# Optimization experiments

Measured on AMD Instinct MI355X. Metric: run time of the kernel, lower is better.

The kernel has to match this reference:

```python
import jax, jax.numpy as jnp
import numpy as np

N_SUPPORT = 16384
EMBED_DIM = 1024
MAX_LEVELS = 4
N_CLASSES = 64


def setup_inputs() -> dict:
    key = jax.random.key(0)
    ks = jax.random.split(key, 12)
    D, L = EMBED_DIM, MAX_LEVELS
    s = 0.02
    return {
        "support_features": jax.random.normal(ks[0], (N_SUPPORT, D), jnp.float32),
        "support_labels": jax.random.randint(ks[1], (N_SUPPORT,), 0, N_CLASSES),
        "sp_w1": jax.random.normal(ks[2], (D, D // 2), jnp.float32) * s,
        "sp_b1": jnp.zeros((D // 2,), jnp.float32),
        "sp_w2": jax.random.normal(ks[3], (D // 2, L), jnp.float32) * s,
        "sp_b2": jnp.zeros((L,), jnp.float32),
        "lvl_emb": jax.random.normal(ks[4], (L, 1), jnp.float32) * s,
        "an_w1": jax.random.normal(ks[5], (L, D + 1, D), jnp.float32) * s,
        "an_b1": jnp.zeros((L, D), jnp.float32),
        "an_gamma": jnp.ones((L, D), jnp.float32),
        "an_beta": jnp.zeros((L, D), jnp.float32),
        "an_w2": jax.random.normal(ks[6], (L, D, D), jnp.float32) * s,
        "an_b2": jnp.zeros((L, D), jnp.float32),
        "fu_w1": jax.random.normal(ks[7], (L * D + L, D), jnp.float32) * s,
        "fu_b1": jnp.zeros((D,), jnp.float32),
        "fu_w2": jax.random.normal(ks[8], (D, D), jnp.float32) * s,
        "fu_b2": jnp.zeros((D,), jnp.float32),
        "n_classes": N_CLASSES,
    }


def _forward(support_features, support_labels, sp_w1, sp_b1, sp_w2, sp_b2,
             lvl_emb, an_w1, an_b1, an_gamma, an_beta, an_w2, an_b2,
             fu_w1, fu_b1, fu_w2, fu_b2, n_classes):
    N, D = support_features.shape
    L = an_w1.shape[0]
    # structure predictor on task context (mean pooled support set)
    task_context = support_features.mean(axis=0)
    h = jax.nn.relu(task_context @ sp_w1 + sp_b1)
    acts = jax.nn.sigmoid(h @ sp_w2 + sp_b2)  # [L]
    ones = jnp.ones((N,), support_features.dtype)
    counts = jax.ops.segment_sum(ones, support_labels, num_segments=n_classes)[:, None]
    counts = jnp.maximum(counts, 1.0)
    # per-level small MLP over ALL support points, then per-class mean via segment_sum
    protos = []
    for l in range(L):  # fixed small loop over structurally distinct level params
        xl = jnp.concatenate([support_features, jnp.broadcast_to(lvl_emb[l], (N, 1))], axis=1)  # [N, D+1]
        hh = xl @ an_w1[l] + an_b1[l]
        mu = hh.mean(axis=-1, keepdims=True)
        var = ((hh - mu) ** 2).mean(axis=-1, keepdims=True)
        hh = (hh - mu) / jnp.sqrt(var + 1e-5) * an_gamma[l] + an_beta[l]  # LayerNorm eps=1e-5
        hh = jax.nn.relu(hh)
        t = hh @ an_w2[l] + an_b2[l]
        protos.append(jax.ops.segment_sum(t, support_labels, num_segments=n_classes) / counts)
    protos = jnp.stack(protos, axis=1)  # [C, L, D]
    # data-dependent gating: pack prototypes of active levels (act > 0.1) to the front,
    # then active weights, then zero padding -- matching torch's concat+pad layout
    mask = acts > 0.1
    mi = mask.astype(jnp.int32)
    slots = jnp.cumsum(mi) - 1          # destination slot of each active level
    k = mi.sum()                        # number of active levels
    slot_or_dump = jnp.where(mask, slots, L)
    packed = jnp.zeros((n_classes, L + 1, D), protos.dtype).at[:, slot_or_dump, :].set(protos)[:, :L, :]
    S = L * D + L
    buf = jnp.zeros((n_classes, S + 1), protos.dtype)
    buf = buf.at[:, : L * D].set(packed.reshape(n_classes, L * D))
    widx = jnp.where(mask, k * D + slots, S)  # weights placed right after the k packed prototypes
    buf = buf.at[:, widx].set(jnp.broadcast_to(acts, (n_classes, L)))
    fusion_input = buf[:, :S]  # [C, L*D + L]
    fused = jax.nn.relu(fusion_input @ fu_w1 + fu_b1) @ fu_w2 + fu_b2  # [C, D]
    raw_mean = jax.ops.segment_sum(support_features, support_labels, num_segments=n_classes) / counts
    prototypes = jnp.where(k > 0, fused, raw_mean)
    level_contributions = jnp.where(mask, acts, 0.0)
    return prototypes, acts, level_contributions


def reference(support_features, support_labels, sp_w1, sp_b1, sp_w2, sp_b2,
              lvl_emb, an_w1, an_b1, an_gamma, an_beta, an_w2, an_b2,
              fu_w1, fu_b1, fu_w2, fu_b2, n_classes):
    return _forward(support_features, support_labels, sp_w1, sp_b1, sp_w2, sp_b2,
                    lvl_emb, an_w1, an_b1, an_gamma, an_beta, an_w2, an_b2,
                    fu_w1, fu_b1, fu_w2, fu_b2, n_classes)
```

## Files before the change

### kernel.cpp

```cpp
#include <hip/hip_runtime.h>
#include <hip/hip_bf16.h>
#include <stdint.h>

#define N_SUP 16384
#define DIM   1024
#define NLV   4
#define NCLS  64
#define NFUSE 4096

typedef __bf16 bf16x8 __attribute__((ext_vector_type(8)));
typedef __bf16 bf16x4 __attribute__((ext_vector_type(4)));
typedef float  f32x4  __attribute__((ext_vector_type(4)));

#define GLOAD_LDS16(g, l) \
    __builtin_amdgcn_global_load_lds((const __attribute__((address_space(1))) void*)(g), \
                                     (__attribute__((address_space(3))) void*)(l), 16, 0, 0)

__global__ __launch_bounds__(256) void k_conv_feat(const float* __restrict__ f,
                                                   __bf16* __restrict__ o) {
    size_t i = ((size_t)blockIdx.x * 256 + threadIdx.x) * 4;
    float4 v = *(const float4*)(f + i);
    union { __bf16 b[4]; uint64_t u; } pk;
    pk.b[0] = (__bf16)v.x; pk.b[1] = (__bf16)v.y;
    pk.b[2] = (__bf16)v.z; pk.b[3] = (__bf16)v.w;
    *(uint64_t*)(o + i) = pk.u;
}

__global__ __launch_bounds__(256) void k_wt(const float* __restrict__ an_w1,
                                            __bf16* __restrict__ w1t) {
    __shared__ float tile[64][65];
    int m = blockIdx.z;
    const float* src = an_w1 + (size_t)m * 1025 * 1024;
    __bf16* dst = w1t + (size_t)m * 1024 * 1024;
    int k0 = blockIdx.x * 64, n0 = blockIdx.y * 64;
    int j = threadIdx.x & 63, i0 = threadIdx.x >> 6;
    #pragma unroll
    for (int ii = 0; ii < 16; ++ii) {
        int i = i0 + ii * 4;
        tile[i][j] = src[(size_t)(k0 + i) * 1024 + n0 + j];
    }
    __syncthreads();
    #pragma unroll
    for (int ii = 0; ii < 16; ++ii) {
        int i = i0 + ii * 4;
        dst[(size_t)(n0 + i) * 1024 + k0 + j] = (__bf16)tile[j][i];
    }
}

__global__ __launch_bounds__(256) void k_eff_b1(const float* __restrict__ an_w1,
                                                const float* __restrict__ an_b1,
                                                const float* __restrict__ lvl_emb,
                                                float* __restrict__ eff) {
    int i = blockIdx.x * 256 + threadIdx.x;
    int l = i >> 10, j = i & 1023;
    eff[i] = an_b1[i] + lvl_emb[l] * an_w1[(size_t)l * 1025 * 1024 + (size_t)1024 * 1024 + j];
}

__global__ __launch_bounds__(1024) void k_rowlist(const int* __restrict__ labels,
                                                  int* __restrict__ rowlist,
                                                  int* __restrict__ gstart,
                                                  int* __restrict__ gcnt,
                                                  float* __restrict__ counts_f) {
    __shared__ int cnt[NCLS];
    __shared__ int sstart[NCLS];
    __shared__ int cur[NCLS];
    int tid = threadIdx.x;
    if (tid < NCLS) cnt[tid] = 0;
    __syncthreads();
    for (int r = tid; r < N_SUP; r += 1024) atomicAdd(&cnt[labels[r]], 1);
    __syncthreads();
    if (tid == 0) {
        int run = 0;
        for (int c = 0; c < NCLS; ++c) { sstart[c] = run; run += cnt[c]; }
    }
    __syncthreads();
    if (tid < NCLS) {
        cur[tid] = sstart[tid];
        gstart[tid] = sstart[tid];
        gcnt[tid] = cnt[tid];
        counts_f[tid] = fmaxf((float)cnt[tid], 1.0f);
    }
    __syncthreads();
    for (int r = tid; r < N_SUP; r += 1024) {
        int pos = atomicAdd(&cur[labels[r]], 1);
        rowlist[pos] = r;
    }
}

__global__ __launch_bounds__(256) void k_gather(const __bf16* __restrict__ X, int ld,
                                                const int* __restrict__ rowlist,
                                                const int* __restrict__ gstart,
                                                const int* __restrict__ gcnt,
                                                const float* __restrict__ counts_f,
                                                float* __restrict__ outp, int div) {
    int c = blockIdx.x;
    int col = blockIdx.y * 256 + threadIdx.x;
    int st = gstart[c], n = gcnt[c];
    float acc = 0.f;
    int i = 0;
    for (; i + 8 <= n; i += 8) {
        int r[8];
        #pragma unroll
        for (int j = 0; j < 8; ++j) r[j] = rowlist[st + i + j];
        float v[8];
        #pragma unroll
        for (int j = 0; j < 8; ++j) v[j] = (float)X[(size_t)r[j] * ld + col];
        #pragma unroll
        for (int j = 0; j < 8; ++j) acc += v[j];
    }
    for (; i < n; ++i) acc += (float)X[(size_t)rowlist[st + i] * ld + col];
    float sc = div ? (1.0f / counts_f[c]) : 1.0f;
    outp[(size_t)c * ld + col] = acc * sc;
}

__global__ __launch_bounds__(256) void k_tasksum(const float* __restrict__ rawsum,
                                                 float* __restrict__ tc) {
    int j = blockIdx.x * 256 + threadIdx.x;
    float t = 0.f;
    for (int c = 0; c < NCLS; ++c) t += rawsum[(size_t)c * DIM + j];
    tc[j] = t * (1.0f / N_SUP);
}

__global__ __launch_bounds__(512) void k_gemv1(const float* __restrict__ tc,
                                               const float* __restrict__ sp_w1,
                                               float* __restrict__ hpre) {
    __shared__ float tcs[64];
    int tid = threadIdx.x;
    int kb = blockIdx.x * 64;
    if (tid < 64) tcs[tid] = tc[kb + tid];
    __syncthreads();
    float acc = 0.f;
    #pragma unroll 8
    for (int k = 0; k < 64; ++k)
        acc += tcs[k] * sp_w1[(size_t)(kb + k) * 512 + tid];
    atomicAdd(&hpre[tid], acc);
}

__global__ __launch_bounds__(512) void k_head_fin(const float* __restrict__ hpre,
                                                  const float* __restrict__ sp_b1,
                                                  const float* __restrict__ sp_w2,
                                                  const float* __restrict__ sp_b2,
                                                  float* __restrict__ headf,
                                                  int* __restrict__ headi,
                                                  float* __restrict__ dout) {
    __shared__ float red[512];
    __shared__ float a4[4];
    int tid = threadIdx.x;
    float hv = hpre[tid] + sp_b1[tid];
    hv = hv > 0.f ? hv : 0.f;
    #pragma unroll
    for (int o = 0; o < 4; ++o) {
        red[tid] = hv * sp_w2[tid * 4 + o];
        __syncthreads();
        for (int st = 256; st > 0; st >>= 1) {
            if (tid < st) red[tid] += red[tid + st];
            __syncthreads();
        }
        if (tid == 0) a4[o] = 1.0f / (1.0f + expf(-(red[0] + sp_b2[o])));
        __syncthreads();
    }
    if (tid == 0) {
        int kk = 0;
        int lvl[4] = {-1, -1, -1, -1};
        for (int l = 0; l < 4; ++l)
            if (a4[l] > 0.1f) { lvl[kk] = l; kk++; }
        headi[0] = kk;
        for (int s = 0; s < 4; ++s) headi[1 + s] = lvl[s];
        for (int l = 0; l < 4; ++l) headf[l] = a4[l];
    }
    if (tid < 4) {
        dout[65536 + tid] = a4[tid];
        dout[65540 + tid] = a4[tid] > 0.1f ? a4[tid] : 0.f;
    }
}

__global__ __launch_bounds__(512, 2) void k_gemm256(const __bf16* __restrict__ A,
                                                    const __bf16* __restrict__ Bt,
                                                    const float* __restrict__ bias,
                                                    __bf16* __restrict__ C,
                                                    int K, int Nn, int NT) {
    __shared__ __bf16 lds[65536];
    const int tid = threadIdx.x;
    const int w   = tid >> 6;
    const int l   = tid & 63;
    const int wr  = w >> 2;
    const int wc  = w & 3;
    const int am  = l & 15;
    const int kg  = l >> 4;
    const size_t bm = (size_t)blockIdx.x * 256;
    const size_t bn = (size_t)blockIdx.y * 256;

    const int srow = w * 8 + (l >> 3);
    const int scol = ((l & 7) ^ (l >> 3)) * 8;
    const __bf16* gA[2][2]; const __bf16* gB[2][2];
    #pragma unroll
    for (int h = 0; h < 2; ++h)
        #pragma unroll
        for (int p = 0; p < 2; ++p) {
            gA[h][p] = A  + (bm + h * 128 + p * 64 + srow) * (size_t)K + scol;
            gB[h][p] = Bt + (bn + h * 128 + p * 64 + srow) * (size_t)K + scol;
        }

    f32x4 acc[8][4] = {};

    #pragma unroll
    for (int h = 0; h < 2; ++h)
        #pragma unroll
        for (int p = 0; p < 2; ++p) {
            GLOAD_LDS16(gA[h][p], lds + h * 8192 + p * 4096 + w * 512);
            GLOAD_LDS16(gB[h][p], lds + 16384 + h * 8192 + p * 4096 + w * 512);
        }

    const int swz = (am & 7) * 8;

#define DSREAD(q, kk, A0, A1, A2, A3, B0, B1) { \
    const int koff_ = (((kk) * 32 + kg * 8) ^ swz); \
    const __bf16* pa_ = lds + cb + wr * 8192 + koff_; \
    const __bf16* pb_ = lds + cb + 16384 + (wc >> 1) * 8192 + ((wc & 1) * 64) * 64 + koff_; \
    A0 = *(const bf16x8*)(pa_ + ((((q) >> 1) * 4 + 0) * 16 + am) * 64); \
    A1 = *(const bf16x8*)(pa_ + ((((q) >> 1) * 4 + 1) * 16 + am) * 64); \
    A2 = *(const bf16x8*)(pa_ + ((((q) >> 1) * 4 + 2) * 16 + am) * 64); \
    A3 = *(const bf16x8*)(pa_ + ((((q) >> 1) * 4 + 3) * 16 + am) * 64); \
    B0 = *(const bf16x8*)(pb_ + ((((q) & 1) * 2 + 0) * 16 + am) * 64); \
    B1 = *(const bf16x8*)(pb_ + ((((q) & 1) * 2 + 1) * 16 + am) * 64); }

#define MFMA8(q, A0, A1, A2, A3, B0, B1) \
    __builtin_amdgcn_s_setprio(1); \
    acc[((q) >> 1) * 4 + 0][((q) & 1) * 2 + 0] = __builtin_amdgcn_mfma_f32_16x16x32_bf16(A0, B0, acc[((q) >> 1) * 4 + 0][((q) & 1) * 2 + 0], 0, 0, 0); \
    acc[((q) >> 1) * 4 + 1][((q) & 1) * 2 + 0] = __builtin_amdgcn_mfma_f32_16x16x32_bf16(A1, B0, acc[((q) >> 1) * 4 + 1][((q) & 1) * 2 + 0], 0, 0, 0); \
    acc[((q) >> 1) * 4 + 2][((q) & 1) * 2 + 0] = __builtin_amdgcn_mfma_f32_16x16x32_bf16(A2, B0, acc[((q) >> 1) * 4 + 2][((q) & 1) * 2 + 0], 0, 0, 0); \
    acc[((q) >> 1) * 4 + 3][((q) & 1) * 2 + 0] = __builtin_amdgcn_mfma_f32_16x16x32_bf16(A3, B0, acc[((q) >> 1) * 4 + 3][((q) & 1) * 2 + 0], 0, 0, 0); \
    acc[((q) >> 1) * 4 + 0][((q) & 1) * 2 + 1] = __builtin_amdgcn_mfma_f32_16x16x32_bf16(A0, B1, acc[((q) >> 1) * 4 + 0][((q) & 1) * 2 + 1], 0, 0, 0); \
    acc[((q) >> 1) * 4 + 1][((q) & 1) * 2 + 1] = __builtin_amdgcn_mfma_f32_16x16x32_bf16(A1, B1, acc[((q) >> 1) * 4 + 1][((q) & 1) * 2 + 1], 0, 0, 0); \
    acc[((q) >> 1) * 4 + 2][((q) & 1) * 2 + 1] = __builtin_amdgcn_mfma_f32_16x16x32_bf16(A2, B1, acc[((q) >> 1) * 4 + 2][((q) & 1) * 2 + 1], 0, 0, 0); \
    acc[((q) >> 1) * 4 + 3][((q) & 1) * 2 + 1] = __builtin_amdgcn_mfma_f32_16x16x32_bf16(A3, B1, acc[((q) >> 1) * 4 + 3][((q) & 1) * 2 + 1], 0, 0, 0); \
    __builtin_amdgcn_s_setprio(0);

    for (int t = 0; t < NT; ++t) {
        const int cb = (t & 1) * 32768;
        const int nb = cb ^ 32768;
        const int tn = (t + 1) * 64;
        const bool more = (t + 1 < NT);
        if (more) {
            GLOAD_LDS16(gA[0][0] + tn, lds + nb + 0 * 4096 + w * 512);
            GLOAD_LDS16(gA[0][1] + tn, lds + nb + 1 * 4096 + w * 512);
            GLOAD_LDS16(gA[1][0] + tn, lds + nb + 8192 + 0 * 4096 + w * 512);
            GLOAD_LDS16(gA[1][1] + tn, lds + nb + 8192 + 1 * 4096 + w * 512);
            asm volatile("s_waitcnt vmcnt(4)" ::: "memory");
        } else {
            asm volatile("s_waitcnt vmcnt(0)" ::: "memory");
        }
        __builtin_amdgcn_s_barrier();

        bf16x8 xa0, xa1, xa2, xa3, xb0, xb1;
        bf16x8 ya0, ya1, ya2, ya3, yb0, yb1;
        DSREAD(0, 0, xa0, xa1, xa2, xa3, xb0, xb1)
        if (more) {
            GLOAD_LDS16(gB[0][0] + tn, lds + nb + 16384 + 0 * 4096 + w * 512);
            GLOAD_LDS16(gB[0][1] + tn, lds + nb + 16384 + 1 * 4096 + w * 512);
        }
        DSREAD(0, 1, ya0, ya1, ya2, ya3, yb0, yb1)
        if (more) {
            GLOAD_LDS16(gB[1][0] + tn, lds + nb + 16384 + 8192 + 0 * 4096 + w * 512);
            GLOAD_LDS16(gB[1][1] + tn, lds + nb + 16384 + 8192 + 1 * 4096 + w * 512);
        }
        MFMA8(0, xa0, xa1, xa2, xa3, xb0, xb1)
        DSREAD(1, 0, xa0, xa1, xa2, xa3, xb0, xb1)
        MFMA8(0, ya0, ya1, ya2, ya3, yb0, yb1)
        DSREAD(1, 1, ya0, ya1, ya2, ya3, yb0, yb1)
        MFMA8(1, xa0, xa1, xa2, xa3, xb0, xb1)
        DSREAD(2, 0, xa0, xa1, xa2, xa3, xb0, xb1)
        MFMA8(1, ya0, ya1, ya2, ya3, yb0, yb1)
        DSREAD(2, 1, ya0, ya1, ya2, ya3, yb0, yb1)
        MFMA8(2, xa0, xa1, xa2, xa3, xb0, xb1)
        DSREAD(3, 0, xa0, xa1, xa2, xa3, xb0, xb1)
        MFMA8(2, ya0, ya1, ya2, ya3, yb0, yb1)
        DSREAD(3, 1, ya0, ya1, ya2, ya3, yb0, yb1)
        MFMA8(3, xa0, xa1, xa2, xa3, xb0, xb1)
        MFMA8(3, ya0, ya1, ya2, ya3, yb0, yb1)
        __builtin_amdgcn_s_barrier();
    }
#undef DSREAD
#undef MFMA8

    const int rbase = kg * 4;
    #pragma unroll
    for (int m = 0; m < 8; ++m) {
        const size_t row = bm + wr * 128 + m * 16 + rbase;
        #pragma unroll
        for (int n = 0; n < 4; ++n) {
            const int col = (int)bn + wc * 64 + n * 16 + am;
            const float bv = bias[col];
            #pragma unroll
            for (int r = 0; r < 4; ++r)
                C[(row + r) * (size_t)Nn + col] = (__bf16)(acc[m][n][r] + bv);
        }
    }
}

__global__ __launch_bounds__(256) void k_gather_ln(const __bf16* __restrict__ hh,
                                                   const float* __restrict__ an_g,
                                                   const float* __restrict__ an_be,
                                                   const int* __restrict__ rowlist,
                                                   const int* __restrict__ gstart,
                                                   const int* __restrict__ gcnt,
                                                   float* __restrict__ gsum) {
    int c = blockIdx.x, lv = blockIdx.y, z = blockIdx.z;
    int tid = threadIdx.x;
    int lane = tid & 63, wv = tid >> 6;
    int col = tid * 4;
    const float* gamma = an_g + lv * 1024;
    const float* beta  = an_be + lv * 1024;
    float g0 = gamma[col], g1 = gamma[col + 1], g2 = gamma[col + 2], g3 = gamma[col + 3];
    float b0 = beta[col],  b1 = beta[col + 1],  b2 = beta[col + 2],  b3 = beta[col + 3];
    int st = gstart[c], n = gcnt[c];
    int per = (n + 7) >> 3;
    int i0 = z * per;
    int i1 = i0 + per < n ? i0 + per : n;
    float a0 = 0.f, a1 = 0.f, a2 = 0.f, a3 = 0.f;
    __shared__ float sred[4], qred[4];
    for (int i = i0; i < i1; ++i) {
        int r = rowlist[st + i];
        bf16x4 v = *(const bf16x4*)(hh + (size_t)r * NFUSE + lv * 1024 + col);
        float x0 = (float)v[0], x1 = (float)v[1], x2 = (float)v[2], x3 = (float)v[3];
        float s = x0 + x1 + x2 + x3;
        float q = x0 * x0 + x1 * x1 + x2 * x2 + x3 * x3;
        s += __shfl_xor(s, 1);  q += __shfl_xor(q, 1);
        s += __shfl_xor(s, 2);  q += __shfl_xor(q, 2);
        s += __shfl_xor(s, 4);  q += __shfl_xor(q, 4);
        s += __shfl_xor(s, 8);  q += __shfl_xor(q, 8);
        s += __shfl_xor(s, 16); q += __shfl_xor(q, 16);
        s += __shfl_xor(s, 32); q += __shfl_xor(q, 32);
        if (lane == 0) { sred[wv] = s; qred[wv] = q; }
        __syncthreads();
        s = sred[0] + sred[1] + sred[2] + sred[3];
        q = qred[0] + qred[1] + qred[2] + qred[3];
        __syncthreads();
        float mu = s * (1.0f / DIM);
        float var = q * (1.0f / DIM) - mu * mu;
        float rstd = rsqrtf(var + 1e-5f);
        float y;
        y = (x0 - mu) * rstd * g0 + b0; a0 += y > 0.f ? y : 0.f;
        y = (x1 - mu) * rstd * g1 + b1; a1 += y > 0.f ? y : 0.f;
        y = (x2 - mu) * rstd * g2 + b2; a2 += y > 0.f ? y : 0.f;
        y = (x3 - mu) * rstd * g3 + b3; a3 += y > 0.f ? y : 0.f;
    }
    if (i0 < i1) {
        size_t o = (size_t)c * NFUSE + lv * 1024 + col;
        atomicAdd(&gsum[o],     a0);
        atomicAdd(&gsum[o + 1], a1);
        atomicAdd(&gsum[o + 2], a2);
        atomicAdd(&gsum[o + 3], a3);
    }
}

__global__ __launch_bounds__(256) void k_build_fi(const float* __restrict__ proto_pre,
                                                  const float* __restrict__ an_b2,
                                                  const int* __restrict__ gcnt,
                                                  const float* __restrict__ counts_f,
                                                  const float* __restrict__ headf,
                                                  const int* __restrict__ headi,
                                                  float* __restrict__ fi) {
    int idx = blockIdx.x * 256 + threadIdx.x;
    if (idx >= 64 * 4160) return;
    int c = idx / 4160, col = idx % 4160;
    int kk = headi[0];
    float v = 0.f;
    if (col < kk * 1024) {
        int s = col >> 10, d = col & 1023;
        int l = headi[1 + s];
        if (gcnt[c] > 0)
            v = proto_pre[((size_t)l * NCLS + c) * DIM + d] / counts_f[c]
                + an_b2[(size_t)l * DIM + d];
    } else if (col < kk * 1024 + kk) {
        int s = col - kk * 1024;
        v = headf[headi[1 + s]];
    }
    fi[idx] = v;
}

__global__ __launch_bounds__(256) void k_fuse_gemm(const float* __restrict__ Abase, int lda, int az,
                                                   const float* __restrict__ Wbase, int wz,
                                                   float* __restrict__ outbase, int oz,
                                                   int K) {
    const float* Afi = Abase + (size_t)blockIdx.z * az;
    const float* W   = Wbase + (size_t)blockIdx.z * wz;
    float* outp      = outbase + (size_t)blockIdx.z * oz;
    __shared__ float fi_lds[64][64];
    int tid = threadIdx.x;
    int tj = tid & 63, tg = tid >> 6;
    int jb = blockIdx.x;
    int k0 = blockIdx.y * 64;
    for (int i = tid; i < 64 * 64; i += 256) {
        int cc = i >> 6, kq = i & 63;
        fi_lds[cc][kq] = (k0 + kq < lda) ? Afi[(size_t)cc * lda + k0 + kq] : 0.f;
    }
    __syncthreads();
    float acc[16] = {};
    #pragma unroll 4
    for (int kq = 0; kq < 64; ++kq) {
        int kg = k0 + kq;
        float wv = (kg < K) ? W[(size_t)kg * 1024 + jb * 64 + tj] : 0.f;
        #pragma unroll
        for (int cc = 0; cc < 16; ++cc)
            acc[cc] += fi_lds[tg * 16 + cc][kq] * wv;
    }
    #pragma unroll
    for (int cc = 0; cc < 16; ++cc)
        atomicAdd(&outp[(size_t)(tg * 16 + cc) * 1024 + jb * 64 + tj], acc[cc]);
}

__global__ __launch_bounds__(256) void k_bias_relu(const float* __restrict__ pre,
                                                   const float* __restrict__ b,
                                                   float* __restrict__ outp) {
    int i = blockIdx.x * 256 + threadIdx.x;
    int j = i & 1023;
    float v = pre[i] + b[j];
    outp[i] = v > 0.f ? v : 0.f;
}

__global__ __launch_bounds__(256) void k_final(const float* __restrict__ pre2,
                                               const float* __restrict__ fu_b2,
                                               const int* __restrict__ headi,
                                               const float* __restrict__ rawsum,
                                               const float* __restrict__ counts_f,
                                               float* __restrict__ dout) {
    int i = blockIdx.x * 256 + threadIdx.x;
    int c = i >> 10, j = i & 1023;
    float v;
    if (headi[0] > 0) v = pre2[i] + fu_b2[j];
    else              v = rawsum[i] / counts_f[c];
    dout[i] = v;
}

extern "C" void kernel_launch(void* const* d_in, const int* in_sizes, int n_in,
                              void* d_out, int out_size, void* d_ws, size_t ws_size,
                              hipStream_t stream) {
    (void)in_sizes; (void)n_in; (void)out_size; (void)ws_size;
    const float* feat    = (const float*)d_in[0];
    const int*   labels  = (const int*)d_in[1];
    const float* sp_w1   = (const float*)d_in[2];
    const float* sp_b1   = (const float*)d_in[3];
    const float* sp_w2   = (const float*)d_in[4];
    const float* sp_b2   = (const float*)d_in[5];
    const float* lvl_emb = (const float*)d_in[6];
    const float* an_w1   = (const float*)d_in[7];
    const float* an_b1   = (const float*)d_in[8];
    const float* an_g    = (const float*)d_in[9];
    const float* an_be   = (const float*)d_in[10];
    const float* an_w2   = (const float*)d_in[11];
    const float* an_b2   = (const float*)d_in[12];
    const float* fu_w1   = (const float*)d_in[13];
    const float* fu_b1   = (const float*)d_in[14];
    const float* fu_w2   = (const float*)d_in[15];
    const float* fu_b2   = (const float*)d_in[16];
    float* dout = (float*)d_out;

    char* p = (char*)d_ws;
    auto alloc = [&](size_t b) { char* r = p; p += (b + 255) & ~(size_t)255; return r; };
    __bf16* featb = (__bf16*)alloc((size_t)N_SUP * DIM * 2);
    __bf16* w1t   = (__bf16*)alloc((size_t)NLV * DIM * DIM * 2);
    __bf16* hh    = (__bf16*)alloc((size_t)N_SUP * NFUSE * 2);
    float*  effb1 = (float*) alloc((size_t)NLV * DIM * 4);
    float*  fi    = (float*) alloc((size_t)64 * 4160 * 4);
    float*  h1    = (float*) alloc((size_t)NCLS * DIM * 4);
    float*  rawsum  = (float*)alloc((size_t)NCLS * DIM * 4);
    float*  tc      = (float*)alloc(DIM * 4);
    int*    rowlist = (int*)  alloc((size_t)N_SUP * 4);
    int*    gstart  = (int*)  alloc(NCLS * 4);
    int*    gcnt    = (int*)  alloc(NCLS * 4);
    float*  counts_f= (float*)alloc(NCLS * 4);
    float*  headf   = (float*)alloc(4 * 4);
    int*    headi   = (int*)  alloc(8 * 4);
    char* z0 = p;
    float*  gsum    = (float*)alloc((size_t)NCLS * NFUSE * 4);
    float*  proto_pre = (float*)alloc((size_t)NLV * NCLS * DIM * 4);
    float*  h1pre   = (float*)alloc((size_t)NCLS * DIM * 4);
    float*  f2pre   = (float*)alloc((size_t)NCLS * DIM * 4);
    float*  hpre    = (float*)alloc(512 * 4);
    size_t zbytes = (size_t)(p - z0);
    hipMemsetAsync(z0, 0, zbytes, stream);

    k_conv_feat<<<N_SUP * DIM / 4 / 256, 256, 0, stream>>>(feat, featb);
    k_wt<<<dim3(16, 16, 4), 256, 0, stream>>>(an_w1, w1t);
    k_eff_b1<<<16, 256, 0, stream>>>(an_w1, an_b1, lvl_emb, effb1);
    k_rowlist<<<1, 1024, 0, stream>>>(labels, rowlist, gstart, gcnt, counts_f);
    k_gather<<<dim3(NCLS, 4), 256, 0, stream>>>(featb, DIM, rowlist, gstart, gcnt,
                                                counts_f, rawsum, 0);
    k_tasksum<<<4, 256, 0, stream>>>(rawsum, tc);
    k_gemv1<<<16, 512, 0, stream>>>(tc, sp_w1, hpre);
    k_head_fin<<<1, 512, 0, stream>>>(hpre, sp_b1, sp_w2, sp_b2, headf, headi, dout);

    k_gemm256<<<dim3(64, 16), 512, 0, stream>>>(featb, w1t, effb1, hh, DIM, NFUSE, DIM / 64);
    k_gather_ln<<<dim3(NCLS, NLV, 8), 256, 0, stream>>>(hh, an_g, an_be,
                                                        rowlist, gstart, gcnt, gsum);
    k_fuse_gemm<<<dim3(16, 16, 4), 256, 0, stream>>>(gsum, NFUSE, 1024,
                                                     an_w2, 1024 * 1024,
                                                     proto_pre, NCLS * DIM, 1024);

    k_build_fi<<<(64 * 4160) / 256, 256, 0, stream>>>(proto_pre, an_b2, gcnt, counts_f,
                                                      headf, headi, fi);
    k_fuse_gemm<<<dim3(16, 65, 1), 256, 0, stream>>>(fi, 4160, 0, fu_w1, 0, h1pre, 0, 4100);
    k_bias_relu<<<NCLS * DIM / 256, 256, 0, stream>>>(h1pre, fu_b1, h1);
    k_fuse_gemm<<<dim3(16, 16, 1), 256, 0, stream>>>(h1, 1024, 0, fu_w2, 0, f2pre, 0, 1024);
    k_final<<<NCLS * DIM / 256, 256, 0, stream>>>(f2pre, fu_b2, headi, rawsum, counts_f, dout);
}
```

Baseline: 370.8 us.

## Restructure GEMM main loop into four quadrant phases and fuse task-sum into gather

The 256x256 GEMM inner loop now splits each k-tile into four quadrant phases. Each phase loads its A/B fragments from LDS and issues 16 MFMAs. Global-to-LDS prefetch loads are spread across these phases with barriers in between, where before the loop interleaved double-buffered register reads. Separately, the task-context column sum is folded into the gather kernel via atomicAdds (buffer moved into the zeroed region), removing one launch. The extra barriers per k-tile and the changed waitcnt placement may cost synchronisation time or raise register pressure.

```diff
diff --git a/kernel.cpp b/kernel.cpp
--- a/kernel.cpp
+++ b/kernel.cpp
@@ -92,7 +92,8 @@
                                                 const int* __restrict__ gstart,
                                                 const int* __restrict__ gcnt,
                                                 const float* __restrict__ counts_f,
-                                                float* __restrict__ outp, int div) {
+                                                float* __restrict__ outp,
+                                                float* __restrict__ tcsum, int div) {
     int c = blockIdx.x;
     int col = blockIdx.y * 256 + threadIdx.x;
     int st = gstart[c], n = gcnt[c];
@@ -111,14 +112,7 @@
     for (; i < n; ++i) acc += (float)X[(size_t)rowlist[st + i] * ld + col];
     float sc = div ? (1.0f / counts_f[c]) : 1.0f;
     outp[(size_t)c * ld + col] = acc * sc;
-}
-
-__global__ __launch_bounds__(256) void k_tasksum(const float* __restrict__ rawsum,
-                                                 float* __restrict__ tc) {
-    int j = blockIdx.x * 256 + threadIdx.x;
-    float t = 0.f;
-    for (int c = 0; c < NCLS; ++c) t += rawsum[(size_t)c * DIM + j];
-    tc[j] = t * (1.0f / N_SUP);
+    if (!div) atomicAdd(&tcsum[col], acc);
 }
 
 __global__ __launch_bounds__(512) void k_gemv1(const float* __restrict__ tc,
@@ -127,7 +121,7 @@
     __shared__ float tcs[64];
     int tid = threadIdx.x;
     int kb = blockIdx.x * 64;
-    if (tid < 64) tcs[tid] = tc[kb + tid];
+    if (tid < 64) tcs[tid] = tc[kb + tid] * (1.0f / N_SUP);
     __syncthreads();
     float acc = 0.f;
     #pragma unroll 8
@@ -213,75 +207,99 @@
 
     const int swz = (am & 7) * 8;
 
-#define DSREAD(q, kk, A0, A1, A2, A3, B0, B1) { \
-    const int koff_ = (((kk) * 32 + kg * 8) ^ swz); \
-    const __bf16* pa_ = lds + cb + wr * 8192 + koff_; \
-    const __bf16* pb_ = lds + cb + 16384 + (wc >> 1) * 8192 + ((wc & 1) * 64) * 64 + koff_; \
-    A0 = *(const bf16x8*)(pa_ + ((((q) >> 1) * 4 + 0) * 16 + am) * 64); \
-    A1 = *(const bf16x8*)(pa_ + ((((q) >> 1) * 4 + 1) * 16 + am) * 64); \
-    A2 = *(const bf16x8*)(pa_ + ((((q) >> 1) * 4 + 2) * 16 + am) * 64); \
-    A3 = *(const bf16x8*)(pa_ + ((((q) >> 1) * 4 + 3) * 16 + am) * 64); \
-    B0 = *(const bf16x8*)(pb_ + ((((q) & 1) * 2 + 0) * 16 + am) * 64); \
-    B1 = *(const bf16x8*)(pb_ + ((((q) & 1) * 2 + 1) * 16 + am) * 64); }
-
-#define MFMA8(q, A0, A1, A2, A3, B0, B1) \
-    __builtin_amdgcn_s_setprio(1); \
-    acc[((q) >> 1) * 4 + 0][((q) & 1) * 2 + 0] = __builtin_amdgcn_mfma_f32_16x16x32_bf16(A0, B0, acc[((q) >> 1) * 4 + 0][((q) & 1) * 2 + 0], 0, 0, 0); \
-    acc[((q) >> 1) * 4 + 1][((q) & 1) * 2 + 0] = __builtin_amdgcn_mfma_f32_16x16x32_bf16(A1, B0, acc[((q) >> 1) * 4 + 1][((q) & 1) * 2 + 0], 0, 0, 0); \
-    acc[((q) >> 1) * 4 + 2][((q) & 1) * 2 + 0] = __builtin_amdgcn_mfma_f32_16x16x32_bf16(A2, B0, acc[((q) >> 1) * 4 + 2][((q) & 1) * 2 + 0], 0, 0, 0); \
-    acc[((q) >> 1) * 4 + 3][((q) & 1) * 2 + 0] = __builtin_amdgcn_mfma_f32_16x16x32_bf16(A3, B0, acc[((q) >> 1) * 4 + 3][((q) & 1) * 2 + 0], 0, 0, 0); \
-    acc[((q) >> 1) * 4 + 0][((q) & 1) * 2 + 1] = __builtin_amdgcn_mfma_f32_16x16x32_bf16(A0, B1, acc[((q) >> 1) * 4 + 0][((q) & 1) * 2 + 1], 0, 0, 0); \
-    acc[((q) >> 1) * 4 + 1][((q) & 1) * 2 + 1] = __builtin_amdgcn_mfma_f32_16x16x32_bf16(A1, B1, acc[((q) >> 1) * 4 + 1][((q) & 1) * 2 + 1], 0, 0, 0); \
-    acc[((q) >> 1) * 4 + 2][((q) & 1) * 2 + 1] = __builtin_amdgcn_mfma_f32_16x16x32_bf16(A2, B1, acc[((q) >> 1) * 4 + 2][((q) & 1) * 2 + 1], 0, 0, 0); \
-    acc[((q) >> 1) * 4 + 3][((q) & 1) * 2 + 1] = __builtin_amdgcn_mfma_f32_16x16x32_bf16(A3, B1, acc[((q) >> 1) * 4 + 3][((q) & 1) * 2 + 1], 0, 0, 0); \
-    __builtin_amdgcn_s_setprio(0);
-
     for (int t = 0; t < NT; ++t) {
         const int cb = (t & 1) * 32768;
         const int nb = cb ^ 32768;
         const int tn = (t + 1) * 64;
         const bool more = (t + 1 < NT);
+        bf16x8 ax[4][2], ay[4][2], bx[2][2], by[2][2];
+        const __bf16* pa = lds + cb + wr * 8192;
+        const __bf16* pb = lds + cb + 16384 + (wc >> 1) * 8192 + ((wc & 1) * 64) * 64;
+
         if (more) {
             GLOAD_LDS16(gA[0][0] + tn, lds + nb + 0 * 4096 + w * 512);
             GLOAD_LDS16(gA[0][1] + tn, lds + nb + 1 * 4096 + w * 512);
+            asm volatile("s_waitcnt vmcnt(2)" ::: "memory");
+        } else {
+            asm volatile("s_waitcnt vmcnt(0)" ::: "memory");
+        }
+        __builtin_amdgcn_s_barrier();
+        #pragma unroll
+        for (int i = 0; i < 4; ++i)
+            #pragma unroll
+            for (int kk = 0; kk < 2; ++kk)
+                ax[i][kk] = *(const bf16x8*)(pa + (i * 16 + am) * 64 + ((kk * 32 + kg * 8) ^ swz));
+        #pragma unroll
+        for (int j = 0; j < 2; ++j)
+            #pragma unroll
+            for (int kk = 0; kk < 2; ++kk)
+                bx[j][kk] = *(const bf16x8*)(pb + (j * 16 + am) * 64 + ((kk * 32 + kg * 8) ^ swz));
+        __builtin_amdgcn_s_setprio(1);
+        #pragma unroll
+        for (int i = 0; i < 4; ++i)
+            #pragma unroll
+            for (int j = 0; j < 2; ++j)
+                #pragma unroll
+                for (int kk = 0; kk < 2; ++kk)
+                    acc[i][j] = __builtin_amdgcn_mfma_f32_16x16x32_bf16(ax[i][kk], bx[j][kk], acc[i][j], 0, 0, 0);
+        __builtin_amdgcn_s_setprio(0);
+        __builtin_amdgcn_s_barrier();
+
+        if (more) {
             GLOAD_LDS16(gA[1][0] + tn, lds + nb + 8192 + 0 * 4096 + w * 512);
             GLOAD_LDS16(gA[1][1] + tn, lds + nb + 8192 + 1 * 4096 + w * 512);
-            asm volatile("s_waitcnt vmcnt(4)" ::: "memory");
-        } else {
-            asm volatile("s_waitcnt vmcnt(0)" ::: "memory");
-        }
+        }
+        #pragma unroll
+        for (int j = 0; j < 2; ++j)
+            #pragma unroll
+            for (int kk = 0; kk < 2; ++kk)
+                by[j][kk] = *(const bf16x8*)(pb + ((2 + j) * 16 + am) * 64 + ((kk * 32 + kg * 8) ^ swz));
+        __builtin_amdgcn_s_setprio(1);
+        #pragma unroll
+        for (int i = 0; i < 4; ++i)
+            #pragma unroll
+            for (int j = 0; j < 2; ++j)
+                #pragma unroll
+                for (int kk = 0; kk < 2; ++kk)
+                    acc[i][2 + j] = __builtin_amdgcn_mfma_f32_16x16x32_bf16(ax[i][kk], by[j][kk], acc[i][2 + j], 0, 0, 0);
+        __builtin_amdgcn_s_setprio(0);
         __builtin_amdgcn_s_barrier();
 
-        bf16x8 xa0, xa1, xa2, xa3, xb0, xb1;
-        bf16x8 ya0, ya1, ya2, ya3, yb0, yb1;
-        DSREAD(0, 0, xa0, xa1, xa2, xa3, xb0, xb1)
         if (more) {
             GLOAD_LDS16(gB[0][0] + tn, lds + nb + 16384 + 0 * 4096 + w * 512);
             GLOAD_LDS16(gB[0][1] + tn, lds + nb + 16384 + 1 * 4096 + w * 512);
         }
-        DSREAD(0, 1, ya0, ya1, ya2, ya3, yb0, yb1)
+        #pragma unroll
+        for (int i = 0; i < 4; ++i)
+            #pragma unroll
+            for (int kk = 0; kk < 2; ++kk)
+                ay[i][kk] = *(const bf16x8*)(pa + ((4 + i) * 16 + am) * 64 + ((kk * 32 + kg * 8) ^ swz));
+        __builtin_amdgcn_s_setprio(1);
+        #pragma unroll
+        for (int i = 0; i < 4; ++i)
+            #pragma unroll
+            for (int j = 0; j < 2; ++j)
+                #pragma unroll
+                for (int kk = 0; kk < 2; ++kk)
+                    acc[4 + i][j] = __builtin_amdgcn_mfma_f32_16x16x32_bf16(ay[i][kk], bx[j][kk], acc[4 + i][j], 0, 0, 0);
+        __builtin_amdgcn_s_setprio(0);
+        __builtin_amdgcn_s_barrier();
+
         if (more) {
             GLOAD_LDS16(gB[1][0] + tn, lds + nb + 16384 + 8192 + 0 * 4096 + w * 512);
             GLOAD_LDS16(gB[1][1] + tn, lds + nb + 16384 + 8192 + 1 * 4096 + w * 512);
         }
-        MFMA8(0, xa0, xa1, xa2, xa3, xb0, xb1)
-        DSREAD(1, 0, xa0, xa1, xa2, xa3, xb0, xb1)
-        MFMA8(0, ya0, ya1, ya2, ya3, yb0, yb1)
-        DSREAD(1, 1, ya0, ya1, ya2, ya3, yb0, yb1)
-        MFMA8(1, xa0, xa1, xa2, xa3, xb0, xb1)
-        DSREAD(2, 0, xa0, xa1, xa2, xa3, xb0, xb1)
-        MFMA8(1, ya0, ya1, ya2, ya3, yb0, yb1)
-        DSREAD(2, 1, ya0, ya1, ya2, ya3, yb0, yb1)
-        MFMA8(2, xa0, xa1, xa2, xa3, xb0, xb1)
-        DSREAD(3, 0, xa0, xa1, xa2, xa3, xb0, xb1)
-        MFMA8(2, ya0, ya1, ya2, ya3, yb0, yb1)
-        DSREAD(3, 1, ya0, ya1, ya2, ya3, yb0, yb1)
-        MFMA8(3, xa0, xa1, xa2, xa3, xb0, xb1)
-        MFMA8(3, ya0, ya1, ya2, ya3, yb0, yb1)
+        __builtin_amdgcn_s_setprio(1);
+        #pragma unroll
+        for (int i = 0; i < 4; ++i)
+            #pragma unroll
+            for (int j = 0; j < 2; ++j)
+                #pragma unroll
+                for (int kk = 0; kk < 2; ++kk)
+                    acc[4 + i][2 + j] = __builtin_amdgcn_mfma_f32_16x16x32_bf16(ay[i][kk], by[j][kk], acc[4 + i][2 + j], 0, 0, 0);
+        __builtin_amdgcn_s_setprio(0);
         __builtin_amdgcn_s_barrier();
     }
-#undef DSREAD
-#undef MFMA8
 
     const int rbase = kg * 4;
     #pragma unroll
@@ -465,7 +483,6 @@
     float*  fi    = (float*) alloc((size_t)64 * 4160 * 4);
     float*  h1    = (float*) alloc((size_t)NCLS * DIM * 4);
     float*  rawsum  = (float*)alloc((size_t)NCLS * DIM * 4);
-    float*  tc      = (float*)alloc(DIM * 4);
     int*    rowlist = (int*)  alloc((size_t)N_SUP * 4);
     int*    gstart  = (int*)  alloc(NCLS * 4);
     int*    gcnt    = (int*)  alloc(NCLS * 4);
@@ -473,6 +490,7 @@
     float*  headf   = (float*)alloc(4 * 4);
     int*    headi   = (int*)  alloc(8 * 4);
     char* z0 = p;
+    float*  tc      = (float*)alloc(DIM * 4);
     float*  gsum    = (float*)alloc((size_t)NCLS * NFUSE * 4);
     float*  proto_pre = (float*)alloc((size_t)NLV * NCLS * DIM * 4);
     float*  h1pre   = (float*)alloc((size_t)NCLS * DIM * 4);
@@ -486,8 +504,7 @@
     k_eff_b1<<<16, 256, 0, stream>>>(an_w1, an_b1, lvl_emb, effb1);
     k_rowlist<<<1, 1024, 0, stream>>>(labels, rowlist, gstart, gcnt, counts_f);
     k_gather<<<dim3(NCLS, 4), 256, 0, stream>>>(featb, DIM, rowlist, gstart, gcnt,
-                                                counts_f, rawsum, 0);
-    k_tasksum<<<4, 256, 0, stream>>>(rawsum, tc);
+                                                counts_f, rawsum, tc, 0);
     k_gemv1<<<16, 512, 0, stream>>>(tc, sp_w1, hpre);
     k_head_fin<<<1, 512, 0, stream>>>(hpre, sp_b1, sp_w2, sp_b2, headf, headi, dout);
 
```

Result: no change. 365.1 us (-1.5%).
